# Optimization experiments

Measured on AMD Instinct MI355X. Metric: run time of the kernel, lower is better.

## Reference

```python
import jax, jax.numpy as jnp
import numpy as np

N = 4_000_000
G = 512          # input grid extent per axis
GP = G // 2      # parent (output) grid extent
SENT = jnp.iinfo(jnp.int32).max  # sort-stable sentinel for padded unique slots


def setup_inputs() -> dict:
    key = jax.random.key(0)
    k1, k2 = jax.random.split(key)
    coords = jax.random.randint(k1, (N, 4), 0, G, dtype=jnp.int32)
    coords = coords.at[:, 0].set(0)  # single batch
    feats = jax.random.normal(k2, (N, 1), dtype=jnp.float32)
    return {"coords": coords, "feats": feats}


def reference(coords, feats):
    # Sparse conv3d, kernel 2x2x2, stride 2, identity (8,1,8) weights ==
    # space-to-depth fold: out[parent, offset_id] = sum of inputs at that
    # offset inside the 2x2x2 block (sum handles duplicate coords like conv).
    b = coords[:, 0]
    xyz = coords[:, 1:]
    parent = xyz >> 1                     # [N,3] output voxel coords
    off = xyz & 1                         # [N,3] position within block
    offset_id = off[:, 0] * 4 + off[:, 1] * 2 + off[:, 2]  # lexicographic (dx,dy,dz)

    # Linearize parent voxel (batch-major) for dedup.
    key_lin = ((b * GP + parent[:, 0]) * GP + parent[:, 1]) * GP + parent[:, 2]

    # Fixed-size (jit-friendly) unique: sorted, padded at end with SENT.
    ukeys = jnp.unique(key_lin, size=N, fill_value=SENT)
    idx = jnp.searchsorted(ukeys, key_lin)  # row in output for each input point

    out_feats = jnp.zeros((N, 8), feats.dtype).at[idx, offset_id].add(feats[:, 0])

    # Decode output coords; mark padded rows with -1.
    kz = ukeys % GP
    ky = (ukeys // GP) % GP
    kx = (ukeys // (GP * GP)) % GP
    kb = ukeys // (GP * GP * GP)
    out_coords = jnp.stack([kb, kx, ky, kz], axis=1).astype(jnp.int32)
    valid = (ukeys != SENT)[:, None]
    out_coords = jnp.where(valid, out_coords, -1)
    return out_coords, out_feats
```

## Files before the change

kernel.cpp:

```cpp
#include <hip/hip_runtime.h>
#include <stdint.h>


static constexpr int      PTS_A  = 2048;
static constexpr int      PTS_B  = 4096;
static constexpr int      NB_A   = 64;
static constexpr int      SHARDS = 8;
static constexpr int      SEGS   = NB_A * SHARDS;
static constexpr uint32_t CAP_A  = 12288;
static constexpr int      BPS_B  = CAP_A / PTS_B;
static constexpr int      NB_B   = 256;
static constexpr int      NBKT   = NB_A * NB_B;
static constexpr uint32_t CAP_B  = 384;
static constexpr int      BKT_PER_CNT = 16;

__device__ __forceinline__ uint32_t make_pk(int4 c) {
    uint32_t key = ((((uint32_t)c.x << 8 | (uint32_t)(c.y >> 1)) << 8 |
                     (uint32_t)(c.z >> 1)) << 8) | (uint32_t)(c.w >> 1);
    uint32_t off = (uint32_t)(c.y & 1) * 4u + (uint32_t)(c.z & 1) * 2u + (uint32_t)(c.w & 1);
    return (key << 3) | off;
}

__device__ __forceinline__ uint32_t wave_incl_scan(uint32_t v, uint32_t lane) {
    #pragma unroll
    for (int d = 1; d < 64; d <<= 1) {
        uint32_t u = __shfl_up(v, d, 64);
        if (lane >= (uint32_t)d) v += u;
    }
    return v;
}

__global__ __launch_bounds__(256) void passA_kernel(const int4* __restrict__ coords,
                                                    const float* __restrict__ feats,
                                                    uint32_t* __restrict__ cursorA,
                                                    uint2* __restrict__ bufA, int n) {
    __shared__ uint32_t hist[NB_A], scx[NB_A], gbase[NB_A];
    __shared__ uint2 stage[PTS_A];
    int t = threadIdx.x, blk = blockIdx.x;
    int base = blk * PTS_A;
    if (t < NB_A) hist[t] = 0;
    __syncthreads();
    uint32_t pk[8]; float f[8]; uint16_t loc[8]; uint8_t bk[8];
    if (base + PTS_A <= n) {
        #pragma unroll
        for (int j = 0; j < 8; j++) {
            int i = base + j * 256 + t;
            pk[j] = make_pk(coords[i]);
            f[j] = feats[i];
            bk[j] = (uint8_t)(pk[j] >> 21);
            loc[j] = (uint16_t)atomicAdd(&hist[bk[j]], 1u);
        }
    } else {
        #pragma unroll
        for (int j = 0; j < 8; j++) {
            int i = base + j * 256 + t;
            if (i < n) {
                pk[j] = make_pk(coords[i]);
                f[j] = feats[i];
                bk[j] = (uint8_t)(pk[j] >> 21);
                loc[j] = (uint16_t)atomicAdd(&hist[bk[j]], 1u);
            } else pk[j] = 0xFFFFFFFFu;
        }
    }
    __syncthreads();
    if (t < NB_A) {
        uint32_t h = hist[t];
        uint32_t incl = wave_incl_scan(h, (uint32_t)t);
        uint32_t excl = incl - h;
        uint32_t shard = (uint32_t)t * SHARDS + (uint32_t)(blk & (SHARDS - 1));
        uint32_t old = atomicAdd(&cursorA[shard * 16], h);
        gbase[t] = shard * CAP_A + old;
        scx[t] = excl;
    }
    __syncthreads();
    #pragma unroll
    for (int j = 0; j < 8; j++)
        if (pk[j] != 0xFFFFFFFFu)
            stage[scx[bk[j]] + loc[j]] = make_uint2(pk[j], __float_as_uint(f[j]));
    int total = (base + PTS_A <= n) ? PTS_A : (n - base);
    __syncthreads();
    for (int s = t; s < total; s += 256) {
        uint2 p = stage[s];
        uint32_t b = p.x >> 21;
        bufA[gbase[b] + ((uint32_t)s - scx[b])] = p;
    }
}

__global__ __launch_bounds__(256) void passB_kernel(const uint2* __restrict__ bufA,
                                                    const uint32_t* __restrict__ cursorA,
                                                    uint32_t* __restrict__ cursorB,
                                                    uint32_t* __restrict__ bufBk,
                                                    float* __restrict__ bufBv) {
    __shared__ uint32_t hist[NB_B], scx[NB_B], gold[NB_B];
    __shared__ uint32_t wsum[4];
    __shared__ uint2 stage[PTS_B];
    int t = threadIdx.x, g = blockIdx.x;
    int sIdx = g / BPS_B, sub = g % BPS_B;
    uint32_t segBase = (uint32_t)sIdx * CAP_A;
    uint32_t segCnt = cursorA[sIdx * 16];
    if (segCnt > CAP_A) segCnt = CAP_A;
    int start = sub * PTS_B;
    int cnt = (int)segCnt - start;
    if (cnt > PTS_B) cnt = PTS_B;
    if (cnt < 0) cnt = 0;
    uint32_t aBase = (uint32_t)(sIdx >> 3) * NB_B;
    hist[t] = 0;
    __syncthreads();
    uint2 pr[16]; uint16_t loc[16]; uint8_t bk[16];
    #pragma unroll
    for (int j = 0; j < 16; j++) {
        int i = j * 256 + t;
        if (i < cnt) {
            pr[j] = bufA[segBase + start + i];
            bk[j] = (uint8_t)((pr[j].x >> 13) & 255u);
            loc[j] = (uint16_t)atomicAdd(&hist[bk[j]], 1u);
        }
    }
    __syncthreads();
    {
        uint32_t lane = (uint32_t)t & 63u, wave = (uint32_t)t >> 6;
        uint32_t h = hist[t];
        uint32_t incl = wave_incl_scan(h, lane);
        if (lane == 63u) wsum[wave] = incl;
        __syncthreads();
        uint32_t add = 0;
        #pragma unroll
        for (uint32_t w = 0; w < 4; w++) if (w < wave) add += wsum[w];
        incl += add;
        uint32_t excl = incl - h;
        gold[t] = atomicAdd(&cursorB[aBase + (uint32_t)t], h);
        scx[t] = excl;
    }
    __syncthreads();
    #pragma unroll
    for (int j = 0; j < 16; j++) {
        int i = j * 256 + t;
        if (i < cnt) stage[scx[bk[j]] + loc[j]] = pr[j];
    }
    __syncthreads();
    for (int s = t; s < cnt; s += 256) {
        uint2 p = stage[s];
        uint32_t b = (p.x >> 13) & 255u;
        uint32_t pos = gold[b] + ((uint32_t)s - scx[b]);
        if (pos < CAP_B) {
            uint32_t o = (aBase + b) * CAP_B + pos;
            bufBk[o] = p.x;
            bufBv[o] = __uint_as_float(p.y);
        }
    }
}

__global__ __launch_bounds__(256) void count_kernel(const uint32_t* __restrict__ bufBk,
                                                    const uint32_t* __restrict__ cursorB,
                                                    uint32_t* __restrict__ ucount,
                                                    uint32_t* __restrict__ bitmapG) {
    __shared__ uint32_t bm[BKT_PER_CNT * 32];
    __shared__ uint32_t cshift[BKT_PER_CNT + 1];
    __shared__ uint32_t ccnt[BKT_PER_CNT];
    int t = threadIdx.x, g = blockIdx.x;
    uint32_t b0 = (uint32_t)g * BKT_PER_CNT;
    for (int i = t; i < BKT_PER_CNT * 32; i += 256) bm[i] = 0;
    if (t < BKT_PER_CNT) {
        uint32_t c = cursorB[b0 + (uint32_t)t]; if (c > CAP_B) c = CAP_B;
        ccnt[t] = c;
    }
    __syncthreads();
    if (t == 0) {
        uint32_t r = 0;
        #pragma unroll
        for (int j = 0; j < BKT_PER_CNT; j++) { cshift[j] = r; r += ccnt[j]; }
        cshift[BKT_PER_CNT] = r;
    }
    __syncthreads();
    uint32_t Tp = cshift[BKT_PER_CNT];
    for (uint32_t i = t; i < Tp; i += 256u) {
        uint32_t bb = 0;
        if (cshift[bb + 8] <= i) bb += 8;
        if (cshift[bb + 4] <= i) bb += 4;
        if (cshift[bb + 2] <= i) bb += 2;
        if (cshift[bb + 1] <= i) bb += 1;
        uint32_t pk = bufBk[(b0 + bb) * CAP_B + (i - cshift[bb])];
        atomicOr(&bm[(bb << 5) + ((pk >> 8) & 31u)], 1u << ((pk >> 3) & 31u));
    }
    __syncthreads();
    if (t < BKT_PER_CNT) {
        uint32_t s = 0;
        #pragma unroll
        for (int w = 0; w < 32; w++) s += (uint32_t)__popc(bm[(t << 5) + w]);
        ucount[b0 + (uint32_t)t] = s;
    }
    for (int i = t; i < BKT_PER_CNT * 32; i += 256)
        bitmapG[(size_t)b0 * 32u + (uint32_t)i] = bm[i];
}

__global__ __launch_bounds__(1024) void scanU_kernel(const uint32_t* __restrict__ ucount,
                                                     uint32_t* __restrict__ baseRank,
                                                     uint32_t* __restrict__ totalOut) {
    __shared__ uint32_t wsum[16];
    int t = threadIdx.x;
    uint32_t lane = (uint32_t)t & 63u, wv = (uint32_t)t >> 6;
    uint32_t v[16]; uint32_t sum = 0;
    #pragma unroll
    for (int j = 0; j < 16; j++) { v[j] = ucount[t * 16 + j]; sum += v[j]; }
    uint32_t incl = wave_incl_scan(sum, lane);
    if (lane == 63u) wsum[wv] = incl;
    __syncthreads();
    if (t < 16) {
        uint32_t s = wsum[t];
        #pragma unroll
        for (int d = 1; d < 16; d <<= 1) {
            uint32_t u = __shfl_up(s, d, 64);
            if (t >= d) s += u;
        }
        wsum[t] = s;
    }
    __syncthreads();
    uint32_t add = (wv > 0) ? wsum[wv - 1] : 0u;
    uint32_t run = add + incl - sum;
    #pragma unroll
    for (int j = 0; j < 16; j++) { baseRank[t * 16 + j] = run; run += v[j]; }
    if (t == 1023) *totalOut = add + incl;
}

__global__ __launch_bounds__(256) void fold_tail_kernel(const uint32_t* __restrict__ bufBk,
                                                        const float* __restrict__ bufBv,
                                                        const uint32_t* __restrict__ cursorB,
                                                        const uint32_t* __restrict__ bitmapG,
                                                        const uint32_t* __restrict__ baseRank,
                                                        const uint32_t* __restrict__ totalPtr,
                                                        float4* __restrict__ outCoords,
                                                        float4* __restrict__ outFeats2, int n) {
    __shared__ float acc[384 * 9];
    __shared__ uint32_t bm[32], wp[32];
    __shared__ uint16_t keylist[384];
    int t = threadIdx.x, b = blockIdx.x;
    uint32_t cnt = cursorB[b]; if (cnt > CAP_B) cnt = CAP_B;
    uint32_t base = (uint32_t)b * CAP_B;
    uint32_t k0 = 0u, k1 = 0u; float v0 = 0.f, v1 = 0.f;
    bool h0 = (uint32_t)t < cnt;
    bool h1 = (uint32_t)t + 256u < cnt;
    if (h0) { k0 = bufBk[base + (uint32_t)t];        v0 = bufBv[base + (uint32_t)t]; }
    if (h1) { k1 = bufBk[base + (uint32_t)t + 256u]; v1 = bufBv[base + (uint32_t)t + 256u]; }
    if (t < 32) bm[t] = bitmapG[(uint32_t)b * 32u + (uint32_t)t];
    for (int i = t; i < 384 * 9; i += 256) acc[i] = 0.f;
    __syncthreads();
    if (t < 32) {
        uint32_t s = (uint32_t)__popc(bm[t]);
        #pragma unroll
        for (int d = 1; d < 32; d <<= 1) {
            uint32_t u = __shfl_up(s, d, 64);
            if ((uint32_t)t >= (uint32_t)d) s += u;
        }
        wp[t] = s;
    }
    __syncthreads();
    for (int k = t; k < 1024; k += 256) {
        uint32_t w = (uint32_t)k >> 5, bit = (uint32_t)k & 31u, word = bm[w];
        if ((word >> bit) & 1u) {
            uint32_t lr = wp[w] - (uint32_t)__popc(word) + (uint32_t)__popc(word & ((1u << bit) - 1u));
            keylist[lr] = (uint16_t)k;
        }
    }
    if (h0) {
        uint32_t kk = (k0 >> 3) & 1023u, w = kk >> 5, bit = kk & 31u;
        uint32_t lr = wp[w] - (uint32_t)__popc(bm[w]) + (uint32_t)__popc(bm[w] & ((1u << bit) - 1u));
        atomicAdd(&acc[lr * 9u + (k0 & 7u)], v0);
    }
    if (h1) {
        uint32_t kk = (k1 >> 3) & 1023u, w = kk >> 5, bit = kk & 31u;
        uint32_t lr = wp[w] - (uint32_t)__popc(bm[w]) + (uint32_t)__popc(bm[w] & ((1u << bit) - 1u));
        atomicAdd(&acc[lr * 9u + (k1 & 7u)], v1);
    }
    __syncthreads();
    int ucnt = (int)wp[31];
    uint32_t rbase = baseRank[b];
    for (int u = t; u < ucnt; u += 256) {
        uint32_t k = keylist[u];
        uint32_t rank = rbase + (uint32_t)u;
        uint32_t key = ((uint32_t)b << 10) | k;
        outCoords[rank] = make_float4((float)(key >> 24), (float)((key >> 16) & 255u),
                                      (float)((key >> 8) & 255u), (float)(key & 255u));
        float4 lo, hi;
        lo.x = acc[u * 9 + 0]; lo.y = acc[u * 9 + 1]; lo.z = acc[u * 9 + 2]; lo.w = acc[u * 9 + 3];
        hi.x = acc[u * 9 + 4]; hi.y = acc[u * 9 + 5]; hi.z = acc[u * 9 + 6]; hi.w = acc[u * 9 + 7];
        outFeats2[(size_t)rank * 2] = lo;
        outFeats2[(size_t)rank * 2 + 1] = hi;
    }
    float4 z4 = make_float4(0.f, 0.f, 0.f, 0.f);
    uint32_t U = *totalPtr;
    uint32_t rows = ((uint32_t)n > U) ? (uint32_t)n - U : 0u;
    uint32_t per = (rows + (uint32_t)gridDim.x - 1u) / (uint32_t)gridDim.x;
    uint32_t s0 = U + (uint32_t)b * per;
    uint32_t s1 = s0 + per; if (s1 > (uint32_t)n) s1 = (uint32_t)n;
    for (uint32_t i = s0 + (uint32_t)t; i < s1; i += 256u) {
        outCoords[i] = make_float4(-1.f, -1.f, -1.f, -1.f);
        outFeats2[(size_t)i * 2] = z4;
        outFeats2[(size_t)i * 2 + 1] = z4;
    }
}

static constexpr uint32_t NKEYS  = 1u << 24;
static constexpr uint32_t NWORDS = 1u << 19;
static constexpr int SCAN_BLOCKS = 512;

__global__ void zero_u4(uint4* __restrict__ p, int count) {
    int i = blockIdx.x * blockDim.x + threadIdx.x;
    int stride = gridDim.x * blockDim.x;
    uint4 z = {0u, 0u, 0u, 0u};
    for (; i < count; i += stride) p[i] = z;
}

__global__ void bytemark_kernel(const int4* __restrict__ coords, uint8_t* __restrict__ bytemap,
                                uint32_t* __restrict__ pkey, int n) {
    int i = blockIdx.x * blockDim.x + threadIdx.x;
    if (i >= n) return;
    uint32_t pk = make_pk(coords[i]);
    bytemap[pk >> 3] = 1;
    pkey[i] = pk;
}

__global__ void build_scan1_kernel(const uint4* __restrict__ bytemap4, uint4* __restrict__ bitmap4,
                                   uint32_t* __restrict__ blockSums) {
    __shared__ uint32_t red[256];
    int t = threadIdx.x;
    int base = blockIdx.x * 256 + t;
    uint4 wb;
    uint32_t* wordOut = (uint32_t*)&wb;
    uint32_t sum = 0;
    #pragma unroll
    for (int j = 0; j < 4; j++) {
        uint4 lo = bytemap4[base * 8 + j * 2];
        uint4 hi = bytemap4[base * 8 + j * 2 + 1];
        const uint32_t* cl = (const uint32_t*)&lo;
        const uint32_t* ch = (const uint32_t*)&hi;
        uint32_t bits = 0;
        #pragma unroll
        for (int k = 0; k < 4; k++)
            bits |= (((cl[k] & 0x01010101u) * 0x10204080u) >> 28) << (4 * k);
        #pragma unroll
        for (int k = 0; k < 4; k++)
            bits |= (((ch[k] & 0x01010101u) * 0x10204080u) >> 28) << (16 + 4 * k);
        wordOut[j] = bits;
        sum += (uint32_t)__popc(bits);
    }
    bitmap4[base] = wb;
    red[t] = sum;
    __syncthreads();
    for (int d = 128; d > 0; d >>= 1) {
        if (t < d) red[t] += red[t + d];
        __syncthreads();
    }
    if (t == 0) blockSums[blockIdx.x] = red[0];
}

__global__ void scan2_kernel(const uint32_t* __restrict__ blockSums, uint32_t* __restrict__ blockOffsets,
                             uint32_t* __restrict__ totalOut) {
    __shared__ uint32_t s[SCAN_BLOCKS];
    int t = threadIdx.x;
    uint32_t v = blockSums[t];
    s[t] = v;
    __syncthreads();
    for (int d = 1; d < SCAN_BLOCKS; d <<= 1) {
        uint32_t x = (t >= d) ? s[t - d] : 0u;
        __syncthreads();
        s[t] += x;
        __syncthreads();
    }
    blockOffsets[t] = s[t] - v;
    if (t == SCAN_BLOCKS - 1) *totalOut = s[t];
}

__global__ void scan3_kernel(const uint4* __restrict__ bitmap4, const uint32_t* __restrict__ blockOffsets,
                             uint4* __restrict__ wordPrefix4) {
    __shared__ uint32_t s[256];
    int t = threadIdx.x;
    int gi = blockIdx.x * 256 + t;
    uint4 w = bitmap4[gi];
    uint32_t p0 = __popc(w.x), p1 = __popc(w.y), p2 = __popc(w.z), p3 = __popc(w.w);
    uint32_t tot = p0 + p1 + p2 + p3;
    s[t] = tot;
    __syncthreads();
    for (int d = 1; d < 256; d <<= 1) {
        uint32_t x = (t >= d) ? s[t - d] : 0u;
        __syncthreads();
        s[t] += x;
        __syncthreads();
    }
    uint32_t excl = s[t] - tot + blockOffsets[blockIdx.x];
    uint4 wp;
    wp.x = excl; wp.y = wp.x + p0; wp.z = wp.y + p1; wp.w = wp.z + p2;
    wordPrefix4[gi] = wp;
}

__global__ void decode_kernel(const uint4* __restrict__ bitmap4, const uint4* __restrict__ wordPrefix4,
                              float4* __restrict__ outCoords) {
    int gi = blockIdx.x * blockDim.x + threadIdx.x;
    if (gi >= (int)(NWORDS / 4)) return;
    uint4 w = bitmap4[gi];
    uint4 wp = wordPrefix4[gi];
    uint32_t words[4] = {w.x, w.y, w.z, w.w};
    uint32_t prefs[4] = {wp.x, wp.y, wp.z, wp.w};
    #pragma unroll
    for (int j = 0; j < 4; j++) {
        uint32_t word = words[j];
        uint32_t rank = prefs[j];
        uint32_t baseKey = ((uint32_t)gi * 4u + (uint32_t)j) * 32u;
        while (word) {
            uint32_t bb = (uint32_t)__ffs(word) - 1u;
            word &= word - 1u;
            uint32_t key = baseKey + bb;
            outCoords[rank++] = make_float4((float)(key >> 24), (float)((key >> 16) & 255u),
                                            (float)((key >> 8) & 255u), (float)(key & 255u));
        }
    }
}

__global__ void tail_fill_kernel(float4* __restrict__ outCoords, float4* __restrict__ outFeats2,
                                 const uint32_t* __restrict__ totalPtr, int n) {
    int i = blockIdx.x * blockDim.x + threadIdx.x;
    if (i >= n) return;
    uint32_t U = *totalPtr;
    if ((uint32_t)i < U) return;
    outCoords[i] = make_float4(-1.f, -1.f, -1.f, -1.f);
    float4 z = make_float4(0.f, 0.f, 0.f, 0.f);
    outFeats2[(size_t)i * 2] = z;
    outFeats2[(size_t)i * 2 + 1] = z;
}

__global__ void scatter_pk_kernel(const uint32_t* __restrict__ pkey, const float* __restrict__ feats,
                                  const uint32_t* __restrict__ bitmap, const uint32_t* __restrict__ wordPrefix,
                                  float* __restrict__ outFeats, int n) {
    int i = blockIdx.x * blockDim.x + threadIdx.x;
    if (i >= n) return;
    uint32_t pk = pkey[i];
    uint32_t key = pk >> 3, off = pk & 7u;
    uint32_t w = key >> 5, bb = key & 31u;
    uint32_t idx = wordPrefix[w] + (uint32_t)__popc(bitmap[w] & ((1u << bb) - 1u));
    atomicAdd(outFeats + (size_t)idx * 8u + off, feats[i]);
}

extern "C" void kernel_launch(void* const* d_in, const int* in_sizes, int n_in,
                              void* d_out, int out_size, void* d_ws, size_t ws_size,
                              hipStream_t stream) {
    const int4* coords = (const int4*)d_in[0];
    const float* feats = (const float*)d_in[1];
    int n = in_sizes[0] / 4;

    float* out = (float*)d_out;
    float4* outCoords = (float4*)out;
    float* outFeats = out + (size_t)n * 4;
    float4* outFeats2 = (float4*)outFeats;

    uint8_t* ws = (uint8_t*)d_ws;
    int ptBlocks = (n + 255) / 256;

    uint32_t* cursorA  = (uint32_t*)ws;
    uint32_t* cursorB  = (uint32_t*)(ws + (32u << 10));
    uint32_t* ucountP  = (uint32_t*)(ws + (128u << 10));
    uint32_t* baseRank = (uint32_t*)(ws + (192u << 10));
    uint32_t* totalU   = (uint32_t*)(ws + (256u << 10));
    uint32_t* bitmapG  = (uint32_t*)(ws + (512u << 10));
    uint2*    bufA  = (uint2*)(ws + (4u << 20));
    uint32_t* bufBk = (uint32_t*)(ws + (4u << 20) + (size_t)SEGS * CAP_A * 8);
    float*    bufBv = (float*)(ws + (4u << 20) + (size_t)SEGS * CAP_A * 8
                               + (size_t)NBKT * CAP_B * 4);
    size_t need2 = (4u << 20) + (size_t)SEGS * CAP_A * 8 + (size_t)NBKT * CAP_B * 8;

    if (ws_size >= need2) {
        hipMemsetAsync(ws, 0, (96u << 10), stream);
        passA_kernel<<<(n + PTS_A - 1) / PTS_A, 256, 0, stream>>>(coords, feats, cursorA, bufA, n);
        passB_kernel<<<SEGS * BPS_B, 256, 0, stream>>>(bufA, cursorA, cursorB, bufBk, bufBv);
        count_kernel<<<NBKT / BKT_PER_CNT, 256, 0, stream>>>(bufBk, cursorB, ucountP, bitmapG);
        scanU_kernel<<<1, 1024, 0, stream>>>(ucountP, baseRank, totalU);
        fold_tail_kernel<<<NBKT, 256, 0, stream>>>(bufBk, bufBv, cursorB, bitmapG, baseRank,
                                                   totalU, outCoords, outFeats2, n);
        return;
    }

    uint32_t* bitmap       = (uint32_t*)ws;
    uint32_t* wordPrefix   = (uint32_t*)(ws + (size_t)NWORDS * 4);
    uint32_t* blockSums    = (uint32_t*)(ws + (size_t)NWORDS * 8);
    uint32_t* blockOffsets = blockSums + SCAN_BLOCKS;
    uint32_t* totalPtr     = blockOffsets + SCAN_BLOCKS;
    uint8_t*  bytemap      = ws + (size_t)NWORDS * 8 + 8192;
    uint32_t* pkey         = (uint32_t*)(bytemap + NKEYS);

    zero_u4<<<2048, 256, 0, stream>>>((uint4*)outFeats, (int)(((size_t)n * 8) / 4));
    zero_u4<<<1024, 256, 0, stream>>>((uint4*)bytemap, (int)(NKEYS / 16));
    bytemark_kernel<<<ptBlocks, 256, 0, stream>>>(coords, bytemap, pkey, n);
    build_scan1_kernel<<<SCAN_BLOCKS, 256, 0, stream>>>((const uint4*)bytemap, (uint4*)bitmap, blockSums);
    scan2_kernel<<<1, SCAN_BLOCKS, 0, stream>>>(blockSums, blockOffsets, totalPtr);
    scan3_kernel<<<SCAN_BLOCKS, 256, 0, stream>>>((const uint4*)bitmap, blockOffsets, (uint4*)wordPrefix);
    decode_kernel<<<(int)(NWORDS / 4 + 255) / 256, 256, 0, stream>>>(
        (const uint4*)bitmap, (const uint4*)wordPrefix, outCoords);
    tail_fill_kernel<<<ptBlocks, 256, 0, stream>>>(outCoords, outFeats2, totalPtr, n);
    scatter_pk_kernel<<<ptBlocks, 256, 0, stream>>>(pkey, feats, bitmap, wordPrefix, outFeats, n);
}
```

Baseline: 341.5 us.

## Build occupancy bitmap in passB via global atomics, shrink count kernel to popcount

Moves construction of the per-bucket parent-occupancy bitmap out of count_kernel into passB, where each scattered point does a global atomicOr into the bitmap. count_kernel then only reads the bitmap and popcounts it with a wave reduction, so it no longer re-reads all bucketed keys from bufBk. The cost is about 4M global atomics during passB plus a larger memset (about 2 MB) to zero the bitmap, and the workspace layout is shifted to fit it.

```diff
diff --git a/kernel.cpp b/kernel.cpp
--- a/kernel.cpp
+++ b/kernel.cpp
@@ -90,7 +90,8 @@
                                                     const uint32_t* __restrict__ cursorA,
                                                     uint32_t* __restrict__ cursorB,
                                                     uint32_t* __restrict__ bufBk,
-                                                    float* __restrict__ bufBv) {
+                                                    float* __restrict__ bufBv,
+                                                    uint32_t* __restrict__ bitmapG) {
     __shared__ uint32_t hist[NB_B], scx[NB_B], gold[NB_B];
     __shared__ uint32_t wsum[4];
     __shared__ uint2 stage[PTS_B];
@@ -147,50 +148,19 @@
             bufBk[o] = p.x;
             bufBv[o] = __uint_as_float(p.y);
         }
-    }
-}
-
-__global__ __launch_bounds__(256) void count_kernel(const uint32_t* __restrict__ bufBk,
-                                                    const uint32_t* __restrict__ cursorB,
-                                                    uint32_t* __restrict__ ucount,
-                                                    uint32_t* __restrict__ bitmapG) {
-    __shared__ uint32_t bm[BKT_PER_CNT * 32];
-    __shared__ uint32_t cshift[BKT_PER_CNT + 1];
-    __shared__ uint32_t ccnt[BKT_PER_CNT];
+        atomicOr(&bitmapG[(size_t)(aBase + b) * 32u + ((p.x >> 8) & 31u)],
+                 1u << ((p.x >> 3) & 31u));
+    }
+}
+
+__global__ __launch_bounds__(256) void count_kernel(const uint2* __restrict__ bitmapG2,
+                                                    uint32_t* __restrict__ ucount) {
     int t = threadIdx.x, g = blockIdx.x;
-    uint32_t b0 = (uint32_t)g * BKT_PER_CNT;
-    for (int i = t; i < BKT_PER_CNT * 32; i += 256) bm[i] = 0;
-    if (t < BKT_PER_CNT) {
-        uint32_t c = cursorB[b0 + (uint32_t)t]; if (c > CAP_B) c = CAP_B;
-        ccnt[t] = c;
-    }
-    __syncthreads();
-    if (t == 0) {
-        uint32_t r = 0;
-        #pragma unroll
-        for (int j = 0; j < BKT_PER_CNT; j++) { cshift[j] = r; r += ccnt[j]; }
-        cshift[BKT_PER_CNT] = r;
-    }
-    __syncthreads();
-    uint32_t Tp = cshift[BKT_PER_CNT];
-    for (uint32_t i = t; i < Tp; i += 256u) {
-        uint32_t bb = 0;
-        if (cshift[bb + 8] <= i) bb += 8;
-        if (cshift[bb + 4] <= i) bb += 4;
-        if (cshift[bb + 2] <= i) bb += 2;
-        if (cshift[bb + 1] <= i) bb += 1;
-        uint32_t pk = bufBk[(b0 + bb) * CAP_B + (i - cshift[bb])];
-        atomicOr(&bm[(bb << 5) + ((pk >> 8) & 31u)], 1u << ((pk >> 3) & 31u));
-    }
-    __syncthreads();
-    if (t < BKT_PER_CNT) {
-        uint32_t s = 0;
-        #pragma unroll
-        for (int w = 0; w < 32; w++) s += (uint32_t)__popc(bm[(t << 5) + w]);
-        ucount[b0 + (uint32_t)t] = s;
-    }
-    for (int i = t; i < BKT_PER_CNT * 32; i += 256)
-        bitmapG[(size_t)b0 * 32u + (uint32_t)i] = bm[i];
+    uint2 w = bitmapG2[(size_t)g * 256u + (uint32_t)t];
+    uint32_t s = (uint32_t)__popc(w.x) + (uint32_t)__popc(w.y);
+    #pragma unroll
+    for (int d = 1; d < 16; d <<= 1) s += __shfl_xor(s, d, 64);
+    if ((t & 15) == 0) ucount[g * BKT_PER_CNT + (t >> 4)] = s;
 }
 
 __global__ __launch_bounds__(1024) void scanU_kernel(const uint32_t* __restrict__ ucount,
@@ -456,10 +426,10 @@
 
     uint32_t* cursorA  = (uint32_t*)ws;
     uint32_t* cursorB  = (uint32_t*)(ws + (32u << 10));
-    uint32_t* ucountP  = (uint32_t*)(ws + (128u << 10));
-    uint32_t* baseRank = (uint32_t*)(ws + (192u << 10));
-    uint32_t* totalU   = (uint32_t*)(ws + (256u << 10));
-    uint32_t* bitmapG  = (uint32_t*)(ws + (512u << 10));
+    uint32_t* bitmapG  = (uint32_t*)(ws + (128u << 10));
+    uint32_t* ucountP  = (uint32_t*)(ws + (2176u << 10));
+    uint32_t* baseRank = (uint32_t*)(ws + (2240u << 10));
+    uint32_t* totalU   = (uint32_t*)(ws + (2304u << 10));
     uint2*    bufA  = (uint2*)(ws + (4u << 20));
     uint32_t* bufBk = (uint32_t*)(ws + (4u << 20) + (size_t)SEGS * CAP_A * 8);
     float*    bufBv = (float*)(ws + (4u << 20) + (size_t)SEGS * CAP_A * 8
@@ -467,10 +437,10 @@
     size_t need2 = (4u << 20) + (size_t)SEGS * CAP_A * 8 + (size_t)NBKT * CAP_B * 8;
 
     if (ws_size >= need2) {
-        hipMemsetAsync(ws, 0, (96u << 10), stream);
+        hipMemsetAsync(ws, 0, (2176u << 10), stream);
         passA_kernel<<<(n + PTS_A - 1) / PTS_A, 256, 0, stream>>>(coords, feats, cursorA, bufA, n);
-        passB_kernel<<<SEGS * BPS_B, 256, 0, stream>>>(bufA, cursorA, cursorB, bufBk, bufBv);
-        count_kernel<<<NBKT / BKT_PER_CNT, 256, 0, stream>>>(bufBk, cursorB, ucountP, bitmapG);
+        passB_kernel<<<SEGS * BPS_B, 256, 0, stream>>>(bufA, cursorA, cursorB, bufBk, bufBv, bitmapG);
+        count_kernel<<<NBKT / BKT_PER_CNT, 256, 0, stream>>>((const uint2*)bitmapG, ucountP);
         scanU_kernel<<<1, 1024, 0, stream>>>(ucountP, baseRank, totalU);
         fold_tail_kernel<<<NBKT, 256, 0, stream>>>(bufBk, bufBv, cursorB, bitmapG, baseRank,
                                                    totalU, outCoords, outFeats2, n);
```

New measurement: 388.3 us. +13.7%, slower.
